# Kernel tuning notes

Hardware: AMD Instinct MI355X
Metric: run time of the kernel (lower is better)

## Reference

```python
import jax, jax.numpy as jnp
import numpy as np

EPS = 1e-5

def setup_inputs() -> dict:
    key = jax.random.key(0)
    k1, k2 = jax.random.split(key)
    x = jax.random.normal(k1, (64, 128, 56, 56), dtype=jnp.float32)
    weight = jax.random.normal(k2, (128, 128, 3, 3), dtype=jnp.float32)  # OIHW
    gamma = jnp.ones((128,), dtype=jnp.float32)   # bn.weight initialized to 1.0
    beta = jnp.zeros((128,), dtype=jnp.float32)   # bn.bias
    return {"x": x, "weight": weight, "gamma": gamma, "beta": beta}

def reference(x, weight, gamma, beta):
    # BinActive / eval-mode sign binarization of activations
    xb = jnp.sign(x)
    # BinaryConv2dKernel: conv with sign-binarized (+/-1) weights, stride 1, pad 1, no bias
    wb = jnp.sign(weight)
    y = jax.lax.conv_general_dilated(
        xb, wb,
        window_strides=(1, 1),
        padding=((1, 1), (1, 1)),
        dimension_numbers=("NCHW", "OIHW", "NCHW"),
    )
    # BatchNorm2d with batch statistics (biased variance), affine gamma/beta
    mean = jnp.mean(y, axis=(0, 2, 3), keepdims=True)           # [1,C,1,1]
    var = jnp.mean((y - mean) ** 2, axis=(0, 2, 3), keepdims=True)
    y_hat = (y - mean) * jax.lax.rsqrt(var + EPS)
    return y_hat * gamma[None, :, None, None] + beta[None, :, None, None]
```

## Files before the change

### kernel.cpp

```cpp
#include <hip/hip_runtime.h>
#include <stdint.h>


#define HH 56
#define WW 56
#define CC 128
#define OO 128
#define NIMG 64
#define PIX (HH*WW)
#define CNT (NIMG*PIX)
#define TOT ((size_t)NIMG*OO*PIX)

#define WS_WPACK 0
#define WS_STATS 18432
#define WS_SS    20480
#define WS_XPACK 32768
#define WS_Y16   3244032
#define WS_NEED  (3244032 + (size_t)TOT*2)

__global__ void pack_w_kernel(const float* __restrict__ w, ulonglong2* __restrict__ wpack) {
    int t = blockIdx.x * 256 + threadIdx.x;
    if (t >= OO * 9) return;
    int o = t / 9, tap = t % 9;
    const float* wp = w + (size_t)o * CC * 9 + tap;
    unsigned long long lo = 0, hi = 0;
    #pragma unroll 4
    for (int c = 0; c < 64; ++c) lo |= (unsigned long long)(wp[c * 9] > 0.0f) << c;
    #pragma unroll 4
    for (int c = 0; c < 64; ++c) hi |= (unsigned long long)(wp[(c + 64) * 9] > 0.0f) << c;
    wpack[t] = make_ulonglong2(lo, hi);
}

__global__ void pack_x_kernel(const float* __restrict__ x, ulonglong2* __restrict__ xpack) {
    int n = blockIdx.y;
    int p = blockIdx.x * 256 + threadIdx.x;
    if (p >= PIX) return;
    const float* xp = x + (size_t)n * CC * PIX + p;
    unsigned long long lo = 0, hi = 0;
    #pragma unroll 8
    for (int c = 0; c < 64; ++c) lo |= (unsigned long long)(xp[(size_t)c * PIX] > 0.0f) << c;
    #pragma unroll 8
    for (int c = 0; c < 64; ++c) hi |= (unsigned long long)(xp[(size_t)(c + 64) * PIX] > 0.0f) << c;
    xpack[n * PIX + p] = make_ulonglong2(lo, hi);
}

template <int MODE>
__global__ __launch_bounds__(256, 2) void conv_kernel(
    const ulonglong2* __restrict__ xpack,
    const ulonglong2* __restrict__ wpack,
    unsigned long long* stats,
    const float2* __restrict__ ss,
    short* __restrict__ y16,
    float* __restrict__ out)
{
    __shared__ ulonglong2 tile[9][58];
    __shared__ int s_sum[256];
    __shared__ int s_sq[256];

    const int og = blockIdx.x;
    const int strip = blockIdx.y;
    const int n = blockIdx.z;
    const int tid = threadIdx.x;
    const int o_idx = tid & 31;
    const int wseg = tid >> 5;
    const int o = og * 32 + o_idx;
    const int w0 = wseg * 7;
    const int h0 = strip * 7;

    {
        const ulonglong2* xp = xpack + n * PIX;
        #pragma unroll
        for (int ii = 0; ii < 3; ++ii) {
            int i = tid + ii * 256;
            if (i < 9 * 58) {
                int r = i / 58, c = i % 58;
                int gr = h0 - 1 + r, gc = c - 1;
                ulonglong2 v = make_ulonglong2(0ULL, 0ULL);
                if (gr >= 0 && gr < HH && gc >= 0 && gc < WW) v = xp[gr * WW + gc];
                tile[r][c] = v;
            }
        }
    }

    ulonglong2 wt[9];
    #pragma unroll
    for (int t = 0; t < 9; ++t) wt[t] = wpack[o * 9 + t];

    int f[9];
    #pragma unroll
    for (int t = 0; t < 9; ++t) f[t] = 128 - 2 * (__popcll(wt[t].x) + __popcll(wt[t].y));
    const int cr0 = f[0] + f[1] + f[2];
    const int cr2 = f[6] + f[7] + f[8];
    const int cc0 = f[0] + f[3] + f[6];
    const int cc2 = f[2] + f[5] + f[8];

    float scale = 0.f, shift = 0.f;
    if (MODE == 2) { float2 v = ss[o]; scale = v.x; shift = v.y; }

    __syncthreads();

    int ysum = 0, ysq = 0;

    for (int hh = 0; hh < 7; ++hh) {
        const int h = h0 + hh;
        int base = 1152;
        if (h == 0) base -= cr0;
        if (h == HH - 1) base -= cr2;
        const int eL = (wseg == 0) ? (cc0 - ((h == 0) ? f[0] : 0) - ((h == HH - 1) ? f[6] : 0)) : 0;
        const int eR = (wseg == 7) ? (cc2 - ((h == 0) ? f[2] : 0) - ((h == HH - 1) ? f[8] : 0)) : 0;

        const ulonglong2* trow = &tile[hh][w0];

        ulonglong2 X[3][3];
        #pragma unroll
        for (int r = 0; r < 3; ++r) {
            X[0][r] = trow[r * 58 + 0];
            X[1][r] = trow[r * 58 + 1];
        }

        size_t obase = ((size_t)(n * OO + o) * HH + h) * WW + w0;

        #pragma unroll
        for (int j = 0; j < 7; ++j) {
            #pragma unroll
            for (int r = 0; r < 3; ++r) X[(j + 2) % 3][r] = trow[r * 58 + j + 2];

            int m0 = 0, m1 = 0, m2 = 0;
            #pragma unroll
            for (int k = 0; k < 3; ++k) {
                ulonglong2 a = X[(j + k) % 3][0];
                m0 += __popcll(a.x ^ wt[k].x) + __popcll(a.y ^ wt[k].y);
                ulonglong2 b = X[(j + k) % 3][1];
                m1 += __popcll(b.x ^ wt[3 + k].x) + __popcll(b.y ^ wt[3 + k].y);
                ulonglong2 c = X[(j + k) % 3][2];
                m2 += __popcll(c.x ^ wt[6 + k].x) + __popcll(c.y ^ wt[6 + k].y);
            }
            int y = base - 2 * (m0 + m1 + m2);
            if (j == 0) y -= eL;
            if (j == 6) y -= eR;

            if (MODE != 2) { ysum += y; ysq += y * y; }
            if (MODE == 1) y16[obase + j] = (short)y;
            if (MODE == 2) out[obase + j] = (float)y * scale + shift;
        }
    }

    if (MODE != 2) {
        s_sum[tid] = ysum;
        s_sq[tid] = ysq;
        __syncthreads();
        if (tid < 32) {
            long long ts = 0, tq = 0;
            #pragma unroll
            for (int k = 0; k < 8; ++k) { ts += s_sum[tid + 32 * k]; tq += s_sq[tid + 32 * k]; }
            int oo = og * 32 + tid;
            atomicAdd(&stats[oo * 2 + 0], (unsigned long long)ts);
            atomicAdd(&stats[oo * 2 + 1], (unsigned long long)tq);
        }
    }
}

__global__ void finalize_kernel(const unsigned long long* __restrict__ stats,
                                const float* __restrict__ gamma,
                                const float* __restrict__ beta,
                                float2* __restrict__ ss) {
    int c = threadIdx.x;
    if (c >= 128) return;
    long long s = (long long)stats[c * 2 + 0];
    long long q = (long long)stats[c * 2 + 1];
    double mean = (double)s / (double)CNT;
    double var = (double)q / (double)CNT - mean * mean;
    double inv = 1.0 / sqrt(var + 1e-5);
    double g = (double)gamma[c];
    float sc = (float)(g * inv);
    float sh = (float)((double)beta[c] - mean * g * inv);
    ss[c] = make_float2(sc, sh);
}

__global__ void norm_kernel(const short* __restrict__ y16,
                            const float2* __restrict__ ss,
                            float* __restrict__ out) {
    size_t g = (size_t)blockIdx.x * 256 + threadIdx.x;
    size_t e = g * 8;
    unsigned int chan = (unsigned int)((e / PIX) & 127);
    float2 v = ss[chan];
    int4 raw = *reinterpret_cast<const int4*>(y16 + e);
    float4 o0, o1;
    o0.x = (float)(short)(raw.x & 0xffff) * v.x + v.y;
    o0.y = (float)(short)(raw.x >> 16)    * v.x + v.y;
    o0.z = (float)(short)(raw.y & 0xffff) * v.x + v.y;
    o0.w = (float)(short)(raw.y >> 16)    * v.x + v.y;
    o1.x = (float)(short)(raw.z & 0xffff) * v.x + v.y;
    o1.y = (float)(short)(raw.z >> 16)    * v.x + v.y;
    o1.z = (float)(short)(raw.w & 0xffff) * v.x + v.y;
    o1.w = (float)(short)(raw.w >> 16)    * v.x + v.y;
    *reinterpret_cast<float4*>(out + e) = o0;
    *reinterpret_cast<float4*>(out + e + 4) = o1;
}

extern "C" void kernel_launch(void* const* d_in, const int* in_sizes, int n_in,
                              void* d_out, int out_size, void* d_ws, size_t ws_size,
                              hipStream_t stream) {
    const float* x     = (const float*)d_in[0];
    const float* wgt   = (const float*)d_in[1];
    const float* gamma = (const float*)d_in[2];
    const float* beta  = (const float*)d_in[3];
    float* out = (float*)d_out;
    char* ws = (char*)d_ws;

    ulonglong2* wpack = (ulonglong2*)(ws + WS_WPACK);
    unsigned long long* stats = (unsigned long long*)(ws + WS_STATS);
    float2* ss = (float2*)(ws + WS_SS);
    ulonglong2* xpack = (ulonglong2*)(ws + WS_XPACK);
    short* y16 = (short*)(ws + WS_Y16);

    hipMemsetAsync(stats, 0, 2048, stream);
    pack_w_kernel<<<5, 256, 0, stream>>>(wgt, wpack);
    pack_x_kernel<<<dim3(13, 64), 256, 0, stream>>>(x, xpack);

    if (ws_size >= WS_NEED) {
        conv_kernel<1><<<dim3(4, 8, 64), 256, 0, stream>>>(xpack, wpack, stats, nullptr, y16, nullptr);
        finalize_kernel<<<1, 128, 0, stream>>>(stats, gamma, beta, ss);
        norm_kernel<<<(unsigned)(TOT / 8 / 256), 256, 0, stream>>>(y16, ss, out);
    } else {
        conv_kernel<0><<<dim3(4, 8, 64), 256, 0, stream>>>(xpack, wpack, stats, nullptr, nullptr, nullptr);
        finalize_kernel<<<1, 128, 0, stream>>>(stats, gamma, beta, ss);
        conv_kernel<2><<<dim3(4, 8, 64), 256, 0, stream>>>(xpack, wpack, stats, ss, nullptr, out);
    }
}
```

Measured before the change: 140.7 us.

## Replace XNOR-popcount binary conv with int8 MFMA implicit GEMM

Activations and weights are now packed as int8 {-1,0,+1} in NHWC/tap-major layout instead of bit-packed words. The convolution becomes an implicit GEMM over 9 taps using 32x32x32 int8 MFMA, with weight tiles double-buffered in shared memory and a 4-row activation strip per block. This moves the XOR/popcount ALU work onto matrix cores and handles zero padding and sign(0)=0 exactly. The trade-off is 8x larger packed activation traffic and a larger workspace (about 25 MB of int8 activations), plus large LDS and accumulator register use.

```diff
diff --git a/kernel.cpp b/kernel.cpp
--- a/kernel.cpp
+++ b/kernel.cpp
@@ -11,151 +11,198 @@
 #define CNT (NIMG*PIX)
 #define TOT ((size_t)NIMG*OO*PIX)
 
-#define WS_WPACK 0
-#define WS_STATS 18432
-#define WS_SS    20480
-#define WS_XPACK 32768
-#define WS_Y16   3244032
-#define WS_NEED  (3244032 + (size_t)TOT*2)
-
-__global__ void pack_w_kernel(const float* __restrict__ w, ulonglong2* __restrict__ wpack) {
+typedef int v4i  __attribute__((ext_vector_type(4)));
+typedef int v16i __attribute__((ext_vector_type(16)));
+
+#define WS_WBT   0
+#define WS_STATS 147456
+#define WS_SS    149504
+#define WS_XI8   151552
+#define WS_Y16   25841664
+#define WS_NEED  (25841664ULL + (size_t)TOT * 2)
+
+__global__ void pack_w_i8(const float* __restrict__ w, char* __restrict__ wbt) {
     int t = blockIdx.x * 256 + threadIdx.x;
-    if (t >= OO * 9) return;
-    int o = t / 9, tap = t % 9;
-    const float* wp = w + (size_t)o * CC * 9 + tap;
-    unsigned long long lo = 0, hi = 0;
-    #pragma unroll 4
-    for (int c = 0; c < 64; ++c) lo |= (unsigned long long)(wp[c * 9] > 0.0f) << c;
-    #pragma unroll 4
-    for (int c = 0; c < 64; ++c) hi |= (unsigned long long)(wp[(c + 64) * 9] > 0.0f) << c;
-    wpack[t] = make_ulonglong2(lo, hi);
-}
-
-__global__ void pack_x_kernel(const float* __restrict__ x, ulonglong2* __restrict__ xpack) {
+    if (t >= 1152) return;
+    int tap = t >> 7, o = t & 127;
+    const float* wp = w + (size_t)o * (CC * 9) + tap;
+    char* dst = wbt + (size_t)t * 128;
+    #pragma unroll
+    for (int chunk = 0; chunk < 8; ++chunk) {
+        v4i v;
+        #pragma unroll
+        for (int wd = 0; wd < 4; ++wd) {
+            unsigned u = 0;
+            #pragma unroll
+            for (int b = 0; b < 4; ++b) {
+                int c = chunk * 16 + wd * 4 + b;
+                float f = wp[c * 9];
+                int s = (f > 0.f) - (f < 0.f);
+                u |= (unsigned)((unsigned char)(char)s) << (8 * b);
+            }
+            v[wd] = (int)u;
+        }
+        *(v4i*)(dst + chunk * 16) = v;
+    }
+}
+
+__global__ void pack_x_i8(const float* __restrict__ x, char* __restrict__ xi8) {
     int n = blockIdx.y;
     int p = blockIdx.x * 256 + threadIdx.x;
     if (p >= PIX) return;
     const float* xp = x + (size_t)n * CC * PIX + p;
-    unsigned long long lo = 0, hi = 0;
-    #pragma unroll 8
-    for (int c = 0; c < 64; ++c) lo |= (unsigned long long)(xp[(size_t)c * PIX] > 0.0f) << c;
-    #pragma unroll 8
-    for (int c = 0; c < 64; ++c) hi |= (unsigned long long)(xp[(size_t)(c + 64) * PIX] > 0.0f) << c;
-    xpack[n * PIX + p] = make_ulonglong2(lo, hi);
+    char* dst = xi8 + ((size_t)n * PIX + p) * CC;
+    #pragma unroll
+    for (int chunk = 0; chunk < 8; ++chunk) {
+        v4i v;
+        #pragma unroll
+        for (int wd = 0; wd < 4; ++wd) {
+            unsigned u = 0;
+            #pragma unroll
+            for (int b = 0; b < 4; ++b) {
+                int c = chunk * 16 + wd * 4 + b;
+                float f = xp[(size_t)c * PIX];
+                int s = (f > 0.f) - (f < 0.f);
+                u |= (unsigned)((unsigned char)(char)s) << (8 * b);
+            }
+            v[wd] = (int)u;
+        }
+        *(v4i*)(dst + chunk * 16) = v;
+    }
 }
 
 template <int MODE>
-__global__ __launch_bounds__(256, 2) void conv_kernel(
-    const ulonglong2* __restrict__ xpack,
-    const ulonglong2* __restrict__ wpack,
-    unsigned long long* stats,
-    const float2* __restrict__ ss,
-    short* __restrict__ y16,
-    float* __restrict__ out)
+__global__ __launch_bounds__(256, 2) void conv_mfma(
+    const char* __restrict__ xi8, const char* __restrict__ wbt,
+    unsigned long long* stats, const float2* __restrict__ ss,
+    short* __restrict__ y16, float* __restrict__ out)
 {
-    __shared__ ulonglong2 tile[9][58];
-    __shared__ int s_sum[256];
-    __shared__ int s_sq[256];
-
-    const int og = blockIdx.x;
-    const int strip = blockIdx.y;
-    const int n = blockIdx.z;
+    __shared__ __align__(16) char Atile[6 * 58 * 128];
+    __shared__ __align__(16) char Btile[2][16384];
+
+    const int strip = blockIdx.x;
+    const int n = blockIdx.y;
     const int tid = threadIdx.x;
-    const int o_idx = tid & 31;
-    const int wseg = tid >> 5;
-    const int o = og * 32 + o_idx;
-    const int w0 = wseg * 7;
-    const int h0 = strip * 7;
+    const int lane = tid & 63;
+    const int wave = tid >> 6;
+    const int ln31 = lane & 31;
+    const int half16 = (lane >> 5) * 16;
+    const int h0 = strip * 4;
 
     {
-        const ulonglong2* xp = xpack + n * PIX;
-        #pragma unroll
-        for (int ii = 0; ii < 3; ++ii) {
-            int i = tid + ii * 256;
-            if (i < 9 * 58) {
-                int r = i / 58, c = i % 58;
-                int gr = h0 - 1 + r, gc = c - 1;
-                ulonglong2 v = make_ulonglong2(0ULL, 0ULL);
-                if (gr >= 0 && gr < HH && gc >= 0 && gc < WW) v = xp[gr * WW + gc];
-                tile[r][c] = v;
-            }
-        }
-    }
-
-    ulonglong2 wt[9];
-    #pragma unroll
-    for (int t = 0; t < 9; ++t) wt[t] = wpack[o * 9 + t];
-
-    int f[9];
-    #pragma unroll
-    for (int t = 0; t < 9; ++t) f[t] = 128 - 2 * (__popcll(wt[t].x) + __popcll(wt[t].y));
-    const int cr0 = f[0] + f[1] + f[2];
-    const int cr2 = f[6] + f[7] + f[8];
-    const int cc0 = f[0] + f[3] + f[6];
-    const int cc2 = f[2] + f[5] + f[8];
-
-    float scale = 0.f, shift = 0.f;
-    if (MODE == 2) { float2 v = ss[o]; scale = v.x; shift = v.y; }
+        const char* xim = xi8 + (size_t)n * PIX * CC;
+        for (int idx = tid; idx < 6 * 448; idx += 256) {
+            int r = idx / 448, c = idx - r * 448;
+            int gr = h0 - 1 + r;
+            v4i v = {0, 0, 0, 0};
+            if (gr >= 0 && gr < HH) v = *(const v4i*)(xim + ((size_t)gr * WW) * CC + c * 16);
+            *(v4i*)(Atile + r * 7424 + 128 + c * 16) = v;
+        }
+        if (tid < 96) {
+            int r = tid >> 4, rem = tid & 15;
+            int off = r * 7424 + ((rem >> 3) ? 57 * 128 : 0) + (rem & 7) * 16;
+            v4i z = {0, 0, 0, 0};
+            *(v4i*)(Atile + off) = z;
+        }
+        #pragma unroll
+        for (int p2 = 0; p2 < 4; ++p2)
+            *(v4i*)(Btile[0] + p2 * 4096 + tid * 16) = *(const v4i*)(wbt + p2 * 4096 + tid * 16);
+    }
+
+    int abase[7];
+    #pragma unroll
+    for (int mt = 0; mt < 7; ++mt) {
+        int q = mt * 32 + ln31;
+        int hh = (q * 586) >> 15;
+        int ww = q - hh * 56;
+        abase[mt] = (hh * 58 + ww) * 128 + half16;
+    }
+    const int bidx = (wave * 32 + ln31) * 128 + half16;
+
+    v16i acc[7];
+    #pragma unroll
+    for (int mt = 0; mt < 7; ++mt) {
+        #pragma unroll
+        for (int i = 0; i < 16; ++i) acc[mt][i] = 0;
+    }
 
     __syncthreads();
 
-    int ysum = 0, ysq = 0;
-
-    for (int hh = 0; hh < 7; ++hh) {
-        const int h = h0 + hh;
-        int base = 1152;
-        if (h == 0) base -= cr0;
-        if (h == HH - 1) base -= cr2;
-        const int eL = (wseg == 0) ? (cc0 - ((h == 0) ? f[0] : 0) - ((h == HH - 1) ? f[6] : 0)) : 0;
-        const int eR = (wseg == 7) ? (cc2 - ((h == 0) ? f[2] : 0) - ((h == HH - 1) ? f[8] : 0)) : 0;
-
-        const ulonglong2* trow = &tile[hh][w0];
-
-        ulonglong2 X[3][3];
-        #pragma unroll
-        for (int r = 0; r < 3; ++r) {
-            X[0][r] = trow[r * 58 + 0];
-            X[1][r] = trow[r * 58 + 1];
-        }
-
-        size_t obase = ((size_t)(n * OO + o) * HH + h) * WW + w0;
-
-        #pragma unroll
-        for (int j = 0; j < 7; ++j) {
-            #pragma unroll
-            for (int r = 0; r < 3; ++r) X[(j + 2) % 3][r] = trow[r * 58 + j + 2];
-
-            int m0 = 0, m1 = 0, m2 = 0;
-            #pragma unroll
-            for (int k = 0; k < 3; ++k) {
-                ulonglong2 a = X[(j + k) % 3][0];
-                m0 += __popcll(a.x ^ wt[k].x) + __popcll(a.y ^ wt[k].y);
-                ulonglong2 b = X[(j + k) % 3][1];
-                m1 += __popcll(b.x ^ wt[3 + k].x) + __popcll(b.y ^ wt[3 + k].y);
-                ulonglong2 c = X[(j + k) % 3][2];
-                m2 += __popcll(c.x ^ wt[6 + k].x) + __popcll(c.y ^ wt[6 + k].y);
-            }
-            int y = base - 2 * (m0 + m1 + m2);
-            if (j == 0) y -= eL;
-            if (j == 6) y -= eR;
-
-            if (MODE != 2) { ysum += y; ysq += y * y; }
-            if (MODE == 1) y16[obase + j] = (short)y;
-            if (MODE == 2) out[obase + j] = (float)y * scale + shift;
-        }
-    }
-
+    #pragma unroll
+    for (int tap = 0; tap < 9; ++tap) {
+        const int buf = tap & 1;
+        v4i pre0, pre1, pre2, pre3;
+        if (tap < 8) {
+            const char* src = wbt + (size_t)(tap + 1) * 16384 + tid * 16;
+            pre0 = *(const v4i*)(src);
+            pre1 = *(const v4i*)(src + 4096);
+            pre2 = *(const v4i*)(src + 8192);
+            pre3 = *(const v4i*)(src + 12288);
+        }
+        const int tapoff = ((tap / 3) * 58 + (tap % 3)) * 128;
+        const char* Bb = Btile[buf] + bidx;
+        #pragma unroll
+        for (int ks = 0; ks < 4; ++ks) {
+            v4i bfrag = *(const v4i*)(Bb + ks * 32);
+            #pragma unroll
+            for (int mt = 0; mt < 7; ++mt) {
+                v4i afrag = *(const v4i*)(Atile + abase[mt] + tapoff + ks * 32);
+                acc[mt] = __builtin_amdgcn_mfma_i32_32x32x32_i8(afrag, bfrag, acc[mt], 0, 0, 0);
+            }
+        }
+        if (tap < 8) {
+            char* dst = Btile[buf ^ 1] + tid * 16;
+            *(v4i*)(dst)         = pre0;
+            *(v4i*)(dst + 4096)  = pre1;
+            *(v4i*)(dst + 8192)  = pre2;
+            *(v4i*)(dst + 12288) = pre3;
+        }
+        __syncthreads();
+    }
+
+    const int o = wave * 32 + ln31;
+    const int hl = lane >> 5;
     if (MODE != 2) {
-        s_sum[tid] = ysum;
-        s_sq[tid] = ysq;
-        __syncthreads();
-        if (tid < 32) {
-            long long ts = 0, tq = 0;
-            #pragma unroll
-            for (int k = 0; k < 8; ++k) { ts += s_sum[tid + 32 * k]; tq += s_sq[tid + 32 * k]; }
-            int oo = og * 32 + tid;
-            atomicAdd(&stats[oo * 2 + 0], (unsigned long long)ts);
-            atomicAdd(&stats[oo * 2 + 1], (unsigned long long)tq);
+        int ysum = 0, ysq = 0;
+        size_t ybase = ((size_t)n * OO + o) * PIX + h0 * WW;
+        #pragma unroll
+        for (int mt = 0; mt < 7; ++mt) {
+            #pragma unroll
+            for (int g = 0; g < 4; ++g) {
+                int y0 = acc[mt][4 * g + 0], y1 = acc[mt][4 * g + 1];
+                int y2 = acc[mt][4 * g + 2], y3 = acc[mt][4 * g + 3];
+                ysum += (y0 + y1) + (y2 + y3);
+                ysq += y0 * y0 + y1 * y1 + y2 * y2 + y3 * y3;
+                if (MODE == 1) {
+                    unsigned lo = ((unsigned)y0 & 0xffffu) | ((unsigned)y1 << 16);
+                    unsigned hi = ((unsigned)y2 & 0xffffu) | ((unsigned)y3 << 16);
+                    int q0 = mt * 32 + g * 8 + hl * 4;
+                    *(uint2*)(y16 + ybase + q0) = make_uint2(lo, hi);
+                }
+            }
+        }
+        int osum = __shfl_xor(ysum, 32);
+        int osq  = __shfl_xor(ysq, 32);
+        ysum += osum; ysq += osq;
+        if (lane < 32) {
+            atomicAdd(&stats[o * 2 + 0], (unsigned long long)(long long)ysum);
+            atomicAdd(&stats[o * 2 + 1], (unsigned long long)(long long)ysq);
+        }
+    } else {
+        float2 v = ss[o];
+        size_t obase = ((size_t)n * OO + o) * PIX + h0 * WW;
+        #pragma unroll
+        for (int mt = 0; mt < 7; ++mt) {
+            #pragma unroll
+            for (int g = 0; g < 4; ++g) {
+                int q0 = mt * 32 + g * 8 + hl * 4;
+                float4 f;
+                f.x = (float)acc[mt][4 * g + 0] * v.x + v.y;
+                f.y = (float)acc[mt][4 * g + 1] * v.x + v.y;
+                f.z = (float)acc[mt][4 * g + 2] * v.x + v.y;
+                f.w = (float)acc[mt][4 * g + 3] * v.x + v.y;
+                *(float4*)(out + obase + q0) = f;
+            }
         }
     }
 }
@@ -208,23 +255,23 @@
     float* out = (float*)d_out;
     char* ws = (char*)d_ws;
 
-    ulonglong2* wpack = (ulonglong2*)(ws + WS_WPACK);
+    char* wbt = ws + WS_WBT;
     unsigned long long* stats = (unsigned long long*)(ws + WS_STATS);
-    float2* ss = (float2*)(ws + WS_SS);
-    ulonglong2* xpack = (ulonglong2*)(ws + WS_XPACK);
+    float2* ssp = (float2*)(ws + WS_SS);
+    char* xi8 = ws + WS_XI8;
     short* y16 = (short*)(ws + WS_Y16);
 
     hipMemsetAsync(stats, 0, 2048, stream);
-    pack_w_kernel<<<5, 256, 0, stream>>>(wgt, wpack);
-    pack_x_kernel<<<dim3(13, 64), 256, 0, stream>>>(x, xpack);
+    pack_w_i8<<<5, 256, 0, stream>>>(wgt, wbt);
+    pack_x_i8<<<dim3(13, 64), 256, 0, stream>>>(x, xi8);
 
     if (ws_size >= WS_NEED) {
-        conv_kernel<1><<<dim3(4, 8, 64), 256, 0, stream>>>(xpack, wpack, stats, nullptr, y16, nullptr);
-        finalize_kernel<<<1, 128, 0, stream>>>(stats, gamma, beta, ss);
-        norm_kernel<<<(unsigned)(TOT / 8 / 256), 256, 0, stream>>>(y16, ss, out);
+        conv_mfma<1><<<dim3(14, 64), 256, 0, stream>>>(xi8, wbt, stats, nullptr, y16, nullptr);
+        finalize_kernel<<<1, 128, 0, stream>>>(stats, gamma, beta, ssp);
+        norm_kernel<<<(unsigned)(TOT / 8 / 256), 256, 0, stream>>>(y16, ssp, out);
     } else {
-        conv_kernel<0><<<dim3(4, 8, 64), 256, 0, stream>>>(xpack, wpack, stats, nullptr, nullptr, nullptr);
-        finalize_kernel<<<1, 128, 0, stream>>>(stats, gamma, beta, ss);
-        conv_kernel<2><<<dim3(4, 8, 64), 256, 0, stream>>>(xpack, wpack, stats, ss, nullptr, out);
-    }
-}
+        conv_mfma<0><<<dim3(14, 64), 256, 0, stream>>>(xi8, wbt, stats, nullptr, nullptr, nullptr);
+        finalize_kernel<<<1, 128, 0, stream>>>(stats, gamma, beta, ssp);
+        conv_mfma<2><<<dim3(14, 64), 256, 0, stream>>>(xi8, wbt, stats, ssp, nullptr, out);
+    }
+}
```

After: 217.9 us. +54.9%, slower.
